# Optimization experiments

Measured on AMD Instinct MI355X. Metric: run time of the kernel, lower is better.

## Reference

```python
import jax, jax.numpy as jnp
import numpy as np

B, S, D = 4, 2048, 1024
E = 8          # num_experts
K = 2          # top-k
H = 2048       # expert_dim


def setup_inputs() -> dict:
    key = jax.random.key(0)
    ks = jax.random.split(key, 7)
    sd = 1.0 / np.sqrt(D)
    sh = 1.0 / np.sqrt(H)
    return {
        "x": jax.random.normal(ks[0], (B, S, D), dtype=jnp.float32),
        "gate_w": jax.random.uniform(ks[1], (D, E), jnp.float32, -sd, sd),
        "gate_b": jax.random.uniform(ks[2], (E,), jnp.float32, -sd, sd),
        "w1": jax.random.uniform(ks[3], (E, D, H), jnp.float32, -sd, sd),
        "b1": jax.random.uniform(ks[4], (E, H), jnp.float32, -sd, sd),
        "w2": jax.random.uniform(ks[5], (E, H, D), jnp.float32, -sh, sh),
        "b2": jax.random.uniform(ks[6], (E, D), jnp.float32, -sh, sh),
    }


def reference(x, gate_w, gate_b, w1, b1, w2, b2):
    T = B * S
    x_flat = x.reshape(T, D)
    # gating
    gate_probs = jax.nn.softmax(x_flat @ gate_w + gate_b, axis=-1)  # [T, E]
    topw, topi = jax.lax.top_k(gate_probs, K)                        # [T, K]
    topw = topw / (jnp.sum(topw, axis=-1, keepdims=True) + 1e-9)
    # dense combine weights [T, E] (top-k indices are unique per token)
    combine = jnp.zeros((T, E), x.dtype).at[jnp.arange(T)[:, None], topi].add(topw)
    # all-experts FFN: relu(x @ W1 + b1) @ W2 + b2 per expert
    h = jax.nn.relu(jnp.einsum('td,edh->eth', x_flat, w1) + b1[:, None, :])  # [E, T, H]
    y = jnp.einsum('eth,ehd->etd', h, w2) + b2[:, None, :]                    # [E, T, D]
    out = jnp.einsum('etd,te->td', y, combine)
    return out.reshape(B, S, D)
```

## Files before the change

### kernel.cpp

```cpp
#include <hip/hip_runtime.h>
#include <hip/hip_bf16.h>
#include <math.h>

#define T_TOK 8192
#define D_DIM 1024
#define E_NUM 8
#define H_DIM 2048

typedef __bf16 bf16;
typedef __bf16 bf16x8 __attribute__((ext_vector_type(8)));
typedef __bf16 bf16x4 __attribute__((ext_vector_type(4)));
typedef float  f32x4  __attribute__((ext_vector_type(4)));

__device__ __forceinline__ void gload_lds16(const void* g, void* s) {
    __builtin_amdgcn_global_load_lds(
        (const __attribute__((address_space(1))) unsigned int*)g,
        (__attribute__((address_space(3))) unsigned int*)s, 16, 0, 0);
}

__global__ void cvt_x_kernel(const float* __restrict__ x, bf16* __restrict__ xb) {
    int i = blockIdx.x * blockDim.x + threadIdx.x;
    const float4* xp = (const float4*)x;
    float4 a = xp[i * 2];
    float4 b = xp[i * 2 + 1];
    bf16x8 o;
    o[0] = (bf16)a.x; o[1] = (bf16)a.y; o[2] = (bf16)a.z; o[3] = (bf16)a.w;
    o[4] = (bf16)b.x; o[5] = (bf16)b.y; o[6] = (bf16)b.z; o[7] = (bf16)b.w;
    *(bf16x8*)(xb + (size_t)i * 8) = o;
}

template <int K, int N>
__global__ void transpose_kernel(const float* __restrict__ W, bf16* __restrict__ Wt) {
    const int e  = blockIdx.z;
    const int kb = blockIdx.y * 32;
    const int nb = blockIdx.x * 32;
    __shared__ float tile[32][33];
    const float* We  = W  + (size_t)e * K * N;
    bf16*        Wte = Wt + (size_t)e * N * K;
    const int tid = threadIdx.x;
    const int r  = tid >> 3;
    const int c4 = (tid & 7) * 4;
    float4 v = *(const float4*)(We + (size_t)(kb + r) * N + nb + c4);
    tile[r][c4 + 0] = v.x; tile[r][c4 + 1] = v.y;
    tile[r][c4 + 2] = v.z; tile[r][c4 + 3] = v.w;
    __syncthreads();
    const int rn = tid >> 3;
    const int k4 = (tid & 7) * 4;
    bf16x4 o;
    o[0] = (bf16)tile[k4 + 0][rn]; o[1] = (bf16)tile[k4 + 1][rn];
    o[2] = (bf16)tile[k4 + 2][rn]; o[3] = (bf16)tile[k4 + 3][rn];
    *(bf16x4*)(Wte + (size_t)(nb + rn) * K + kb + k4) = o;
}

__global__ __launch_bounds__(256) void gating_kernel(
    const float* __restrict__ x, const float* __restrict__ gw,
    const float* __restrict__ gb,
    int* __restrict__ eIdx, float* __restrict__ wgt) {
    __shared__ float xs[4 * D_DIM];
    const int tid  = threadIdx.x;
    const int wave = tid >> 6;
    const int lane = tid & 63;
    {
        const float4* src = (const float4*)(x + (size_t)blockIdx.x * 4 * D_DIM);
        float4* dst = (float4*)xs;
#pragma unroll
        for (int k = 0; k < 4; k++) dst[tid + k * 256] = src[tid + k * 256];
    }
    __syncthreads();

    const int e = lane & 7;
    const int s = lane >> 3;
    const float* xw = xs + wave * D_DIM;
    double acc_a = 0.0, acc_b = 0.0;
#pragma unroll 8
    for (int i = 0; i < 128; i += 2) {
        int d0 = i * 8 + s;
        int d1 = (i + 1) * 8 + s;
        acc_a += (double)xw[d0] * (double)gw[d0 * 8 + e];
        acc_b += (double)xw[d1] * (double)gw[d1 * 8 + e];
    }
    double acc = acc_a + acc_b;
    acc += __shfl_xor(acc, 8, 64);
    acc += __shfl_xor(acc, 16, 64);
    acc += __shfl_xor(acc, 32, 64);
    double lg[E_NUM];
#pragma unroll
    for (int k = 0; k < E_NUM; k++) lg[k] = __shfl(acc, k, 64);

    if (lane == 0) {
        int token = blockIdx.x * 4 + wave;
        double v[E_NUM], p[E_NUM];
        double mx = -1e300;
#pragma unroll
        for (int k = 0; k < E_NUM; k++) { v[k] = lg[k] + (double)gb[k]; mx = fmax(mx, v[k]); }
        double sum = 0.0;
#pragma unroll
        for (int k = 0; k < E_NUM; k++) { p[k] = exp(v[k] - mx); sum += p[k]; }
        int i0 = 0; double p0 = p[0];
#pragma unroll
        for (int k = 1; k < E_NUM; k++) if (p[k] > p0) { p0 = p[k]; i0 = k; }
        int i1 = -1; double p1 = -1.0;
#pragma unroll
        for (int k = 0; k < E_NUM; k++) if (k != i0 && p[k] > p1) { p1 = p[k]; i1 = k; }
        double q0 = p0 / sum, q1 = p1 / sum;
        double sw = q0 + q1 + 1e-9;
        eIdx[token * 2]     = i0;
        eIdx[token * 2 + 1] = i1;
        wgt[token * 2]      = (float)(q0 / sw);
        wgt[token * 2 + 1]  = (float)(q1 / sw);
    }
}

__global__ void count_kernel(const int* __restrict__ eIdx, int* __restrict__ counts) {
    __shared__ int bc[E_NUM];
    const int tid = threadIdx.x;
    if (tid < E_NUM) bc[tid] = 0;
    __syncthreads();
    int2 ev = *(const int2*)(eIdx + (size_t)blockIdx.x * 512 + tid * 2);
    atomicAdd(&bc[ev.x], 1);
    atomicAdd(&bc[ev.y], 1);
    __syncthreads();
    if (tid < E_NUM) atomicAdd(&counts[tid], bc[tid]);
}

__global__ void scan_kernel(const int* __restrict__ counts, int* __restrict__ offsets) {
    if (threadIdx.x == 0) {
        int s = 0;
        for (int e = 0; e < E_NUM; e++) { offsets[e] = s; s += counts[e]; }
    }
}

__global__ void scatter_kernel(const int* __restrict__ eIdx, const int* __restrict__ offsets,
                               int* __restrict__ fill, int* __restrict__ rowIdx,
                               int* __restrict__ slot) {
    __shared__ int bc[E_NUM];
    __shared__ int bbase[E_NUM];
    __shared__ int bcur[E_NUM];
    const int tid = threadIdx.x;
    if (tid < E_NUM) { bc[tid] = 0; bcur[tid] = 0; }
    __syncthreads();
    int t0 = blockIdx.x * 512 + tid * 2;
    int4 ev = *(const int4*)(eIdx + (size_t)t0 * 2);
    atomicAdd(&bc[ev.x], 1);
    atomicAdd(&bc[ev.y], 1);
    atomicAdd(&bc[ev.z], 1);
    atomicAdd(&bc[ev.w], 1);
    __syncthreads();
    if (tid < E_NUM) bbase[tid] = atomicAdd(&fill[tid], bc[tid]);
    __syncthreads();
    int p0 = atomicAdd(&bcur[ev.x], 1);
    int r0 = offsets[ev.x] + bbase[ev.x] + p0;
    rowIdx[r0] = t0; slot[t0 * 2] = r0;
    int p1 = atomicAdd(&bcur[ev.y], 1);
    int r1 = offsets[ev.y] + bbase[ev.y] + p1;
    rowIdx[r1] = t0; slot[t0 * 2 + 1] = r1;
    int p2 = atomicAdd(&bcur[ev.z], 1);
    int r2 = offsets[ev.z] + bbase[ev.z] + p2;
    rowIdx[r2] = t0 + 1; slot[(t0 + 1) * 2] = r2;
    int p3 = atomicAdd(&bcur[ev.w], 1);
    int r3 = offsets[ev.w] + bbase[ev.w] + p3;
    rowIdx[r3] = t0 + 1; slot[(t0 + 1) * 2 + 1] = r3;
}

template <int KD, int ND, bool RELU, bool GATHER>
__global__ __launch_bounds__(256, 2) void moe_gemm_kernel(
    const bf16* __restrict__ A, const bf16* __restrict__ Bt,
    const float* __restrict__ bias, bf16* __restrict__ Out,
    const int* __restrict__ counts, const int* __restrict__ offsets,
    const int* __restrict__ rowIdx) {
    const int e  = blockIdx.z;
    const int Ne = counts[e];
    const int rb = blockIdx.y;
    if (rb * 128 >= Ne) return;
    const int base = offsets[e];
    const int n0   = blockIdx.x * 128;
    const bf16*  Be = Bt + (size_t)e * KD * ND;
    const float* be = bias + (size_t)e * ND;

    __shared__ bf16 As[128 * 32];
    __shared__ bf16 Bs[128 * 32];

    const int tid  = threadIdx.x;
    const int wave = tid >> 6;
    const int lane = tid & 63;

    const int srow  = wave * 16 + (lane >> 2);
    const int skoff = (lane & 3) * 8;
    int m0g = rb * 128 + srow;      if (m0g >= Ne) m0g = Ne - 1;
    int m1g = rb * 128 + 64 + srow; if (m1g >= Ne) m1g = Ne - 1;
    const bf16 *aA0, *aA1;
    if (GATHER) {
        aA0 = A + (size_t)rowIdx[base + m0g] * KD + skoff;
        aA1 = A + (size_t)rowIdx[base + m1g] * KD + skoff;
    } else {
        aA0 = A + (size_t)(base + m0g) * KD + skoff;
        aA1 = A + (size_t)(base + m1g) * KD + skoff;
    }
    const bf16* bB0 = Be + (size_t)(n0 + srow) * KD + skoff;
    const bf16* bB1 = Be + (size_t)(n0 + 64 + srow) * KD + skoff;
    char* dstA0 = (char*)As + wave * 1024;
    char* dstA1 = (char*)As + 4096 + wave * 1024;
    char* dstB0 = (char*)Bs + wave * 1024;
    char* dstB1 = (char*)Bs + 4096 + wave * 1024;

    const int wm = (wave >> 1) * 64;
    const int wn = (wave & 1) * 64;
    const int lrow = lane & 15;
    const int quad = lane >> 4;

    f32x4 acc[4][4] = {};

    for (int k0 = 0; k0 < KD; k0 += 32) {
        gload_lds16(aA0 + k0, dstA0);
        gload_lds16(aA1 + k0, dstA1);
        gload_lds16(bB0 + k0, dstB0);
        gload_lds16(bB1 + k0, dstB1);
        __syncthreads();

        bf16x8 af[4], bfv[4];
#pragma unroll
        for (int t4 = 0; t4 < 4; t4++)
            af[t4] = *(const bf16x8*)&As[(wm + t4 * 16 + lrow) * 32 + quad * 8];
#pragma unroll
        for (int t4 = 0; t4 < 4; t4++)
            bfv[t4] = *(const bf16x8*)&Bs[(wn + t4 * 16 + lrow) * 32 + quad * 8];
#pragma unroll
        for (int ti = 0; ti < 4; ti++)
#pragma unroll
            for (int tj = 0; tj < 4; tj++)
                acc[ti][tj] = __builtin_amdgcn_mfma_f32_16x16x32_bf16(
                    af[ti], bfv[tj], acc[ti][tj], 0, 0, 0);
        __syncthreads();
    }

#pragma unroll
    for (int ti = 0; ti < 4; ti++) {
        int rloc = wm + ti * 16 + quad * 4;
#pragma unroll
        for (int tj = 0; tj < 4; tj++) {
            int gcol = n0 + wn + tj * 16 + lrow;
            float bb = be[gcol];
#pragma unroll
            for (int r = 0; r < 4; r++) {
                int grow = rb * 128 + rloc + r;
                if (grow < Ne) {
                    float v = acc[ti][tj][r] + bb;
                    if (RELU) v = v > 0.f ? v : 0.f;
                    Out[(size_t)(base + grow) * ND + gcol] = (bf16)v;
                }
            }
        }
    }
}

__global__ void combine_kernel(const bf16* __restrict__ Yb, const int* __restrict__ slot,
                               const float* __restrict__ wgt, float* __restrict__ out) {
    int t = blockIdx.x;
    int d = threadIdx.x * 4;
    int s0 = slot[t * 2], s1 = slot[t * 2 + 1];
    float w0 = wgt[t * 2], w1 = wgt[t * 2 + 1];
    bf16x4 y0 = *(const bf16x4*)(Yb + (size_t)s0 * D_DIM + d);
    bf16x4 y1 = *(const bf16x4*)(Yb + (size_t)s1 * D_DIM + d);
    float4 o;
    o.x = w0 * (float)y0[0] + w1 * (float)y1[0];
    o.y = w0 * (float)y0[1] + w1 * (float)y1[1];
    o.z = w0 * (float)y0[2] + w1 * (float)y1[2];
    o.w = w0 * (float)y0[3] + w1 * (float)y1[3];
    *(float4*)(out + (size_t)t * D_DIM + d) = o;
}

extern "C" void kernel_launch(void* const* d_in, const int* in_sizes, int n_in,
                              void* d_out, int out_size, void* d_ws, size_t ws_size,
                              hipStream_t stream) {
    const float* x  = (const float*)d_in[0];
    const float* gw = (const float*)d_in[1];
    const float* gb = (const float*)d_in[2];
    const float* w1 = (const float*)d_in[3];
    const float* b1 = (const float*)d_in[4];
    const float* w2 = (const float*)d_in[5];
    const float* b2 = (const float*)d_in[6];
    float* out = (float*)d_out;

    char* ws = (char*)d_ws;
    int*   counts = (int*)ws;
    int*   fill   = (int*)(ws + 32);
    int*   offs   = (int*)(ws + 64);
    int*   eIdx   = (int*)(ws + 256);
    float* wgt    = (float*)(ws + 256 + 65536);
    int*   slot   = (int*)(ws + 256 + 2 * 65536);
    int*   rowIdx = (int*)(ws + 256 + 3 * 65536);
    bf16*  Xb  = (bf16*)(ws + 262400);
    bf16*  Hb  = (bf16*)(ws + 17039616);
    bf16*  W2t = (bf16*)(ws + 84148480);
    bf16*  W1t = (bf16*)(ws + 117702912);
    bf16*  Yb  = W1t;

    if (ws_size < (size_t)151257344) return;

    hipMemsetAsync(ws, 0, 64, stream);
    cvt_x_kernel<<<(T_TOK * D_DIM) / (256 * 8), 256, 0, stream>>>(x, Xb);
    transpose_kernel<D_DIM, H_DIM>
        <<<dim3(H_DIM / 32, D_DIM / 32, E_NUM), 256, 0, stream>>>(w1, W1t);
    transpose_kernel<H_DIM, D_DIM>
        <<<dim3(D_DIM / 32, H_DIM / 32, E_NUM), 256, 0, stream>>>(w2, W2t);
    gating_kernel<<<T_TOK / 4, 256, 0, stream>>>(x, gw, gb, eIdx, wgt);
    count_kernel<<<T_TOK * 2 / 512, 256, 0, stream>>>(eIdx, counts);
    scan_kernel<<<1, 64, 0, stream>>>(counts, offs);
    scatter_kernel<<<T_TOK / 512, 256, 0, stream>>>(eIdx, offs, fill, rowIdx, slot);
    moe_gemm_kernel<D_DIM, H_DIM, true, true>
        <<<dim3(H_DIM / 128, T_TOK / 128, E_NUM), 256, 0, stream>>>(
            Xb, W1t, b1, Hb, counts, offs, rowIdx);
    moe_gemm_kernel<H_DIM, D_DIM, false, false>
        <<<dim3(D_DIM / 128, T_TOK / 128, E_NUM), 256, 0, stream>>>(
            Hb, W2t, b2, Yb, counts, offs, (const int*)nullptr);
    combine_kernel<<<T_TOK, 256, 0, stream>>>(Yb, slot, wgt, out);
}
```

Baseline: 472.1 us.

## Fuse top-k combine into second expert GEMM via atomics and widen K tile with swizzle

The separate combine kernel is removed. The second expert GEMM now scales each output row by its routing weight and atomically adds it into the fp32 output, which is zeroed beforehand, and the scatter step stores a per-slot weight for this. The GEMM K-tile also grows from 32 to 64, with an XOR-swizzled LDS layout meant to avoid bank conflicts. This removes the bf16 Y round-trip and one launch, but adds scattered fp32 atomics and an output memset. Atomic summation order is nondeterministic.

```diff
diff --git a/kernel.cpp b/kernel.cpp
--- a/kernel.cpp
+++ b/kernel.cpp
@@ -131,8 +131,8 @@
 }
 
 __global__ void scatter_kernel(const int* __restrict__ eIdx, const int* __restrict__ offsets,
-                               int* __restrict__ fill, int* __restrict__ rowIdx,
-                               int* __restrict__ slot) {
+                               const float* __restrict__ wgt, int* __restrict__ fill,
+                               int* __restrict__ rowIdx, float* __restrict__ wslot) {
     __shared__ int bc[E_NUM];
     __shared__ int bbase[E_NUM];
     __shared__ int bcur[E_NUM];
@@ -141,6 +141,7 @@
     __syncthreads();
     int t0 = blockIdx.x * 512 + tid * 2;
     int4 ev = *(const int4*)(eIdx + (size_t)t0 * 2);
+    float4 wv = *(const float4*)(wgt + (size_t)t0 * 2);
     atomicAdd(&bc[ev.x], 1);
     atomicAdd(&bc[ev.y], 1);
     atomicAdd(&bc[ev.z], 1);
@@ -150,24 +151,25 @@
     __syncthreads();
     int p0 = atomicAdd(&bcur[ev.x], 1);
     int r0 = offsets[ev.x] + bbase[ev.x] + p0;
-    rowIdx[r0] = t0; slot[t0 * 2] = r0;
+    rowIdx[r0] = t0;     wslot[r0] = wv.x;
     int p1 = atomicAdd(&bcur[ev.y], 1);
     int r1 = offsets[ev.y] + bbase[ev.y] + p1;
-    rowIdx[r1] = t0; slot[t0 * 2 + 1] = r1;
+    rowIdx[r1] = t0;     wslot[r1] = wv.y;
     int p2 = atomicAdd(&bcur[ev.z], 1);
     int r2 = offsets[ev.z] + bbase[ev.z] + p2;
-    rowIdx[r2] = t0 + 1; slot[(t0 + 1) * 2] = r2;
+    rowIdx[r2] = t0 + 1; wslot[r2] = wv.z;
     int p3 = atomicAdd(&bcur[ev.w], 1);
     int r3 = offsets[ev.w] + bbase[ev.w] + p3;
-    rowIdx[r3] = t0 + 1; slot[(t0 + 1) * 2 + 1] = r3;
-}
-
-template <int KD, int ND, bool RELU, bool GATHER>
+    rowIdx[r3] = t0 + 1; wslot[r3] = wv.w;
+}
+
+template <int KD, int ND, bool RELU, bool GATHER, bool COMBINE>
 __global__ __launch_bounds__(256, 2) void moe_gemm_kernel(
     const bf16* __restrict__ A, const bf16* __restrict__ Bt,
     const float* __restrict__ bias, bf16* __restrict__ Out,
     const int* __restrict__ counts, const int* __restrict__ offsets,
-    const int* __restrict__ rowIdx) {
+    const int* __restrict__ rowIdx, const float* __restrict__ wslot,
+    float* __restrict__ outF) {
     const int e  = blockIdx.z;
     const int Ne = counts[e];
     const int rb = blockIdx.y;
@@ -177,62 +179,76 @@
     const bf16*  Be = Bt + (size_t)e * KD * ND;
     const float* be = bias + (size_t)e * ND;
 
-    __shared__ bf16 As[128 * 32];
-    __shared__ bf16 Bs[128 * 32];
+    __shared__ bf16 As[128 * 64];
+    __shared__ bf16 Bs[128 * 64];
 
     const int tid  = threadIdx.x;
     const int wave = tid >> 6;
     const int lane = tid & 63;
 
-    const int srow  = wave * 16 + (lane >> 2);
-    const int skoff = (lane & 3) * 8;
-    int m0g = rb * 128 + srow;      if (m0g >= Ne) m0g = Ne - 1;
-    int m1g = rb * 128 + 64 + srow; if (m1g >= Ne) m1g = Ne - 1;
-    const bf16 *aA0, *aA1;
-    if (GATHER) {
-        aA0 = A + (size_t)rowIdx[base + m0g] * KD + skoff;
-        aA1 = A + (size_t)rowIdx[base + m1g] * KD + skoff;
-    } else {
-        aA0 = A + (size_t)(base + m0g) * KD + skoff;
-        aA1 = A + (size_t)(base + m1g) * KD + skoff;
-    }
-    const bf16* bB0 = Be + (size_t)(n0 + srow) * KD + skoff;
-    const bf16* bB1 = Be + (size_t)(n0 + 64 + srow) * KD + skoff;
-    char* dstA0 = (char*)As + wave * 1024;
-    char* dstA1 = (char*)As + 4096 + wave * 1024;
-    char* dstB0 = (char*)Bs + wave * 1024;
-    char* dstB1 = (char*)Bs + 4096 + wave * 1024;
+    const int sr = lane >> 3;
+    const int cg = (lane & 7) ^ sr;
+    const bf16* aP[4];
+    const bf16* bP[4];
+#pragma unroll
+    for (int i = 0; i < 4; i++) {
+        int m = rb * 128 + i * 32 + wave * 8 + sr;
+        if (m >= Ne) m = Ne - 1;
+        int arow = GATHER ? rowIdx[base + m] : (base + m);
+        aP[i] = A + (size_t)arow * KD + cg * 8;
+        int n = n0 + i * 32 + wave * 8 + sr;
+        bP[i] = Be + (size_t)n * KD + cg * 8;
+    }
 
     const int wm = (wave >> 1) * 64;
     const int wn = (wave & 1) * 64;
     const int lrow = lane & 15;
     const int quad = lane >> 4;
+    const int r7   = lrow & 7;
 
     f32x4 acc[4][4] = {};
 
-    for (int k0 = 0; k0 < KD; k0 += 32) {
-        gload_lds16(aA0 + k0, dstA0);
-        gload_lds16(aA1 + k0, dstA1);
-        gload_lds16(bB0 + k0, dstB0);
-        gload_lds16(bB1 + k0, dstB1);
+    for (int k0 = 0; k0 < KD; k0 += 64) {
+#pragma unroll
+        for (int i = 0; i < 4; i++) {
+            gload_lds16(aP[i] + k0, (char*)As + i * 4096 + wave * 1024);
+            gload_lds16(bP[i] + k0, (char*)Bs + i * 4096 + wave * 1024);
+        }
         __syncthreads();
 
-        bf16x8 af[4], bfv[4];
-#pragma unroll
-        for (int t4 = 0; t4 < 4; t4++)
-            af[t4] = *(const bf16x8*)&As[(wm + t4 * 16 + lrow) * 32 + quad * 8];
-#pragma unroll
-        for (int t4 = 0; t4 < 4; t4++)
-            bfv[t4] = *(const bf16x8*)&Bs[(wn + t4 * 16 + lrow) * 32 + quad * 8];
+#pragma unroll
+        for (int h = 0; h < 2; h++) {
+            bf16x8 af[4], bfv[4];
+#pragma unroll
+            for (int t4 = 0; t4 < 4; t4++) {
+                int pc = (quad + h * 4) ^ r7;
+                af[t4]  = *(const bf16x8*)&As[(wm + t4 * 16 + lrow) * 64 + pc * 8];
+                bfv[t4] = *(const bf16x8*)&Bs[(wn + t4 * 16 + lrow) * 64 + pc * 8];
+            }
+#pragma unroll
+            for (int ti = 0; ti < 4; ti++)
+#pragma unroll
+                for (int tj = 0; tj < 4; tj++)
+                    acc[ti][tj] = __builtin_amdgcn_mfma_f32_16x16x32_bf16(
+                        af[ti], bfv[tj], acc[ti][tj], 0, 0, 0);
+        }
+        __syncthreads();
+    }
+
+    int   tokr[4][4];
+    float wr[4][4];
+    if (COMBINE) {
 #pragma unroll
         for (int ti = 0; ti < 4; ti++)
 #pragma unroll
-            for (int tj = 0; tj < 4; tj++)
-                acc[ti][tj] = __builtin_amdgcn_mfma_f32_16x16x32_bf16(
-                    af[ti], bfv[tj], acc[ti][tj], 0, 0, 0);
-        __syncthreads();
-    }
-
+            for (int r = 0; r < 4; r++) {
+                int grow = rb * 128 + wm + ti * 16 + quad * 4 + r;
+                if (grow < Ne) {
+                    tokr[ti][r] = rowIdx[base + grow];
+                    wr[ti][r]   = wslot[base + grow];
+                }
+            }
+    }
 #pragma unroll
     for (int ti = 0; ti < 4; ti++) {
         int rloc = wm + ti * 16 + quad * 4;
@@ -246,27 +262,15 @@
                 if (grow < Ne) {
                     float v = acc[ti][tj][r] + bb;
                     if (RELU) v = v > 0.f ? v : 0.f;
-                    Out[(size_t)(base + grow) * ND + gcol] = (bf16)v;
+                    if (COMBINE) {
+                        atomicAdd(&outF[(size_t)tokr[ti][r] * ND + gcol], v * wr[ti][r]);
+                    } else {
+                        Out[(size_t)(base + grow) * ND + gcol] = (bf16)v;
+                    }
                 }
             }
         }
     }
-}
-
-__global__ void combine_kernel(const bf16* __restrict__ Yb, const int* __restrict__ slot,
-                               const float* __restrict__ wgt, float* __restrict__ out) {
-    int t = blockIdx.x;
-    int d = threadIdx.x * 4;
-    int s0 = slot[t * 2], s1 = slot[t * 2 + 1];
-    float w0 = wgt[t * 2], w1 = wgt[t * 2 + 1];
-    bf16x4 y0 = *(const bf16x4*)(Yb + (size_t)s0 * D_DIM + d);
-    bf16x4 y1 = *(const bf16x4*)(Yb + (size_t)s1 * D_DIM + d);
-    float4 o;
-    o.x = w0 * (float)y0[0] + w1 * (float)y1[0];
-    o.y = w0 * (float)y0[1] + w1 * (float)y1[1];
-    o.z = w0 * (float)y0[2] + w1 * (float)y1[2];
-    o.w = w0 * (float)y0[3] + w1 * (float)y1[3];
-    *(float4*)(out + (size_t)t * D_DIM + d) = o;
 }
 
 extern "C" void kernel_launch(void* const* d_in, const int* in_sizes, int n_in,
@@ -286,18 +290,18 @@
     int*   fill   = (int*)(ws + 32);
     int*   offs   = (int*)(ws + 64);
     int*   eIdx   = (int*)(ws + 256);
-    float* wgt    = (float*)(ws + 256 + 65536);
-    int*   slot   = (int*)(ws + 256 + 2 * 65536);
-    int*   rowIdx = (int*)(ws + 256 + 3 * 65536);
+    float* wgt    = (float*)(ws + 65792);
+    float* wslot  = (float*)(ws + 131328);
+    int*   rowIdx = (int*)(ws + 196864);
     bf16*  Xb  = (bf16*)(ws + 262400);
     bf16*  Hb  = (bf16*)(ws + 17039616);
     bf16*  W2t = (bf16*)(ws + 84148480);
     bf16*  W1t = (bf16*)(ws + 117702912);
-    bf16*  Yb  = W1t;
 
     if (ws_size < (size_t)151257344) return;
 
     hipMemsetAsync(ws, 0, 64, stream);
+    hipMemsetAsync(out, 0, (size_t)T_TOK * D_DIM * 4, stream);
     cvt_x_kernel<<<(T_TOK * D_DIM) / (256 * 8), 256, 0, stream>>>(x, Xb);
     transpose_kernel<D_DIM, H_DIM>
         <<<dim3(H_DIM / 32, D_DIM / 32, E_NUM), 256, 0, stream>>>(w1, W1t);
@@ -306,12 +310,11 @@
     gating_kernel<<<T_TOK / 4, 256, 0, stream>>>(x, gw, gb, eIdx, wgt);
     count_kernel<<<T_TOK * 2 / 512, 256, 0, stream>>>(eIdx, counts);
     scan_kernel<<<1, 64, 0, stream>>>(counts, offs);
-    scatter_kernel<<<T_TOK / 512, 256, 0, stream>>>(eIdx, offs, fill, rowIdx, slot);
-    moe_gemm_kernel<D_DIM, H_DIM, true, true>
+    scatter_kernel<<<T_TOK / 512, 256, 0, stream>>>(eIdx, offs, wgt, fill, rowIdx, wslot);
+    moe_gemm_kernel<D_DIM, H_DIM, true, true, false>
         <<<dim3(H_DIM / 128, T_TOK / 128, E_NUM), 256, 0, stream>>>(
-            Xb, W1t, b1, Hb, counts, offs, rowIdx);
-    moe_gemm_kernel<H_DIM, D_DIM, false, false>
+            Xb, W1t, b1, Hb, counts, offs, rowIdx, (const float*)nullptr, (float*)nullptr);
+    moe_gemm_kernel<H_DIM, D_DIM, false, false, true>
         <<<dim3(D_DIM / 128, T_TOK / 128, E_NUM), 256, 0, stream>>>(
-            Hb, W2t, b2, Yb, counts, offs, (const int*)nullptr);
-    combine_kernel<<<T_TOK, 256, 0, stream>>>(Yb, slot, wgt, out);
-}
+            Hb, W2t, b2, (bf16*)nullptr, counts, offs, rowIdx, wslot, out);
+}
```

New measurement: 477.2 us. Within noise of the previous version (+1.1%).
